# Kernel optimization log

Hardware: AMD Instinct MI355X
Metric: run time of the kernel (lower is better)

## Reference

```python
import jax, jax.numpy as jnp
import numpy as np
import math

NUM_HEADS = 8
EPS = 1e-12  # torch F.normalize eps


def setup_inputs() -> dict:
    key = jax.random.key(0)
    ks = jax.random.split(key, 11)
    b, t, l, c = 2, 8, 1024, 256
    s = 0.02
    return {
        "q": jax.random.normal(ks[0], (b, t, l, c), jnp.float32),
        "k": jax.random.normal(ks[1], (b, t, l, c), jnp.float32),
        "v": jax.random.normal(ks[2], (b, t, l, c), jnp.float32),
        "Wq": jax.random.normal(ks[3], (c, c), jnp.float32) * s,
        "bq": jax.random.normal(ks[4], (c,), jnp.float32) * s,
        "Wk": jax.random.normal(ks[5], (c, c), jnp.float32) * s,
        "bk": jax.random.normal(ks[6], (c,), jnp.float32) * s,
        "Wv": jax.random.normal(ks[7], (c, c), jnp.float32) * s,
        "bv": jax.random.normal(ks[8], (c,), jnp.float32) * s,
        "Wm": jax.random.normal(ks[9], (c, c), jnp.float32) * s,
        "bm": jax.random.normal(ks[10], (c,), jnp.float32) * s,
    }


def _proj_norm(x, W, bias, h, d):
    # Linear (torch: x @ W.T + b), split heads, L2-normalize over head_dim.
    b_, t_, l_, c_ = x.shape
    y = (x @ W.T + bias).reshape(b_, t_, l_, h, d).transpose(0, 1, 3, 2, 4)  # [b,t,h,l,d]
    n = jnp.maximum(jnp.linalg.norm(y, axis=-1, keepdims=True), EPS)
    return y / n


def reference(q, k, v, Wq, bq, Wk, bk, Wv, bv, Wm, bm):
    b, t, l, c = q.shape
    h = NUM_HEADS
    d = c // h
    shortcut = q
    qn = _proj_norm(q, Wq, bq, h, d)  # [b,t,h,l,d]
    kn = _proj_norm(k, Wk, bk, h, d)
    vn = _proj_norm(v, Wv, bv, h, d)
    scores = jnp.einsum('bthqd,bthkd->bthqk', qn, kn) / math.sqrt(d)
    attn = jax.nn.softmax(scores, axis=-1)
    x = jnp.einsum('bthqk,bthkd->bthqd', attn, vn)  # [b,t,h,l,d]
    x = x.transpose(0, 1, 3, 2, 4).reshape(b, t, l, c)
    return x @ Wm.T + bm + shortcut
```

## Files before the change

### kernel.cpp

```cpp
#include <hip/hip_runtime.h>
#include <hip/hip_bf16.h>


#define NTOK  16384
#define CDIM  256
#define LSEQ  1024
#define HEADS 8
#define DHEAD 32

typedef _Float16 f16;
typedef __attribute__((ext_vector_type(2))) _Float16 f16x2;
typedef __attribute__((ext_vector_type(4))) _Float16 f16x4;
typedef __attribute__((ext_vector_type(8))) _Float16 f16x8;
typedef __attribute__((ext_vector_type(4))) float f32x4;
typedef __attribute__((ext_vector_type(16))) float f32x16;

#define QSCALE (0.17677669529663687f * 1.4426950408889634f)

__device__ __forceinline__ f16x2 pkcvt(float a, float b) {
  auto r = __builtin_amdgcn_cvt_pkrtz(a, b);
  union { decltype(r) in; f16x2 out; } u;
  u.in = r;
  return u.out;
}

__device__ __forceinline__ f16x4 pack4(float4 a) {
  union { f16x4 v; f16x2 h[2]; } u;
  u.h[0] = pkcvt(a.x, a.y);
  u.h[1] = pkcvt(a.z, a.w);
  return u.v;
}

__global__ __launch_bounds__(256)
void cvt_w_kernel(const float* __restrict__ Wq, const float* __restrict__ Wk,
                  const float* __restrict__ Wv, const float* __restrict__ Wm,
                  f16* __restrict__ dst) {
  const int m = blockIdx.x >> 6;
  const float* src = (m == 0) ? Wq : (m == 1) ? Wk : (m == 2) ? Wv : Wm;
  const int base = (blockIdx.x & 63) * 1024 + threadIdx.x * 4;
  const int och = base >> 8, ch = base & 255;
  float4 a = *(const float4*)(src + base);
  *(f16x4*)(dst + m * 65536 + (ch >> 5) * 8192 + och * 32 + (ch & 31)) =
      pack4(a);
}

#define PKKB 1288

__global__ __launch_bounds__(256, 2)
void proj_mfma_kernel(const float* __restrict__ xq, const float* __restrict__ xk,
                      const float* __restrict__ xv, const f16* __restrict__ w16,
                      const float* __restrict__ bq, const float* __restrict__ bk,
                      const float* __restrict__ bv,
                      f16* __restrict__ qn, f16* __restrict__ kn,
                      f16* __restrict__ vt) {
  __shared__ f16 xl[8 * PKKB];
  const int which = blockIdx.y;
  const float* x    = (which == 0) ? xq : (which == 1) ? xk : xv;
  const float* bias = (which == 0) ? bq : (which == 1) ? bk : bv;
  const f16* W      = w16 + which * 65536;
  f16* out          = (which == 0) ? qn : (which == 1) ? kn : vt;
  const float scale = (which == 0) ? QSCALE : 1.0f;
  const bool transposed = (which == 2);

  const int tid = threadIdx.x;
  const int wave = tid >> 6, lane = tid & 63;
  const int quad = lane >> 4, l16 = lane & 15;
  const int tokbase = blockIdx.x * 32;
  const int wbase = wave * 64;

  {
    const int c16 = lane;
#pragma unroll
    for (int r = 0; r < 8; ++r) {
      const int tok = r * 4 + wave;
      float4 a = *(const float4*)(x + (size_t)(tokbase + tok) * CDIM + c16 * 4);
      *(f16x4*)(&xl[(c16 >> 3) * PKKB + tok * 40 + (c16 & 7) * 4]) = pack4(a);
    }
  }
  __syncthreads();

  f32x4 acc[4][2];
#pragma unroll
  for (int mt = 0; mt < 4; ++mt)
#pragma unroll
    for (int nt = 0; nt < 2; ++nt) acc[mt][nt] = (f32x4){0.f, 0.f, 0.f, 0.f};

#pragma unroll
  for (int kk = 0; kk < 8; ++kk) {
    f16x8 af[4];
#pragma unroll
    for (int mt = 0; mt < 4; ++mt)
      af[mt] = *(const f16x8*)(W + kk * 8192 + (wbase + mt * 16 + l16) * 32 +
                               quad * 8);
    f16x8 bf0 = *(const f16x8*)(&xl[kk * PKKB + l16 * 40 + quad * 8]);
    f16x8 bf1 = *(const f16x8*)(&xl[kk * PKKB + (16 + l16) * 40 + quad * 8]);
#pragma unroll
    for (int mt = 0; mt < 4; ++mt) {
      acc[mt][0] = __builtin_amdgcn_mfma_f32_16x16x32_f16(af[mt], bf0,
                                                          acc[mt][0], 0, 0, 0);
      acc[mt][1] = __builtin_amdgcn_mfma_f32_16x16x32_f16(af[mt], bf1,
                                                          acc[mt][1], 0, 0, 0);
    }
  }

  const int bt = tokbase >> 10, l0 = tokbase & 1023;
#pragma unroll
  for (int hh = 0; hh < 2; ++hh) {
    const int h = wave * 2 + hh;
    const size_t hb = (size_t)(bt * HEADS + h) * (LSEQ * DHEAD);
    float4 b0 = *(const float4*)(bias + wbase + hh * 32 + quad * 4);
    float4 b1 = *(const float4*)(bias + wbase + hh * 32 + 16 + quad * 4);
#pragma unroll
    for (int nt = 0; nt < 2; ++nt) {
      f32x4 a0 = acc[hh * 2 + 0][nt];
      f32x4 a1 = acc[hh * 2 + 1][nt];
      float v0[4], v1[4];
      v0[0] = a0[0] + b0.x; v0[1] = a0[1] + b0.y;
      v0[2] = a0[2] + b0.z; v0[3] = a0[3] + b0.w;
      v1[0] = a1[0] + b1.x; v1[1] = a1[1] + b1.y;
      v1[2] = a1[2] + b1.z; v1[3] = a1[3] + b1.w;
      float ss = 0.f;
#pragma unroll
      for (int r = 0; r < 4; ++r) ss += v0[r] * v0[r] + v1[r] * v1[r];
      ss += __shfl_xor(ss, 16);
      ss += __shfl_xor(ss, 32);
      const float inv = scale / fmaxf(sqrtf(ss), 1e-12f);
      const int tok_l = l0 + nt * 16 + l16;
      if (!transposed) {
        f16x4 o0, o1;
#pragma unroll
        for (int r = 0; r < 4; ++r) {
          o0[r] = (f16)(v0[r] * inv);
          o1[r] = (f16)(v1[r] * inv);
        }
        *(f16x4*)(out + hb + (size_t)tok_l * DHEAD + quad * 4) = o0;
        *(f16x4*)(out + hb + (size_t)tok_l * DHEAD + 16 + quad * 4) = o1;
      } else {
        const int tcol = (tok_l & ~12) | ((tok_l & 4) << 1) | ((tok_l & 8) >> 1);
#pragma unroll
        for (int r = 0; r < 4; ++r) {
          out[hb + (size_t)(quad * 4 + r) * LSEQ + tcol] = (f16)(v0[r] * inv);
          out[hb + (size_t)(16 + quad * 4 + r) * LSEQ + tcol] = (f16)(v1[r] * inv);
        }
      }
    }
  }
}

#define TKROW 40
#define TVROW 72

__global__ __launch_bounds__(256, 4)
void attn_mfma_kernel(const f16* __restrict__ qn,
                      const f16* __restrict__ kn,
                      const f16* __restrict__ vt,
                      f16* __restrict__ xo) {
  __shared__ f16 kl[2][64 * TKROW];
  __shared__ f16 vl[2][32 * TVROW];
  const int tid  = threadIdx.x;
  const int wave = tid >> 6, lane = tid & 63;
  const int l32 = lane & 31, hi = lane >> 5;
  const int wid = (blockIdx.x & 7) * 128 + (blockIdx.x >> 3);
  const int bth = wid >> 3;
  const int qbase = ((wid & 7) << 7) + wave * 32;
  const size_t hb = (size_t)bth * (LSEQ * DHEAD);

  const f16* qp = qn + hb + (size_t)(qbase + l32) * DHEAD + hi * 8;
  const f16x8 qf0 = *(const f16x8*)qp;
  const f16x8 qf1 = *(const f16x8*)(qp + 16);

  const int krow_w = wave * 16 + (lane >> 2), kcol = (lane & 3) * 8;
  const int vrow_w = wave * 8 + (lane >> 3), vcol = (lane & 7) * 8;
  const f16* gK = kn + hb + (size_t)krow_w * DHEAD + kcol;
  const f16* gV = vt + hb + (size_t)vrow_w * LSEQ + vcol;
  const int lK = krow_w * TKROW + kcol;
  const int lV = vrow_w * TVROW + vcol;

  f32x16 oacc, z16;
#pragma unroll
  for (int r = 0; r < 16; ++r) { oacc[r] = 0.f; z16[r] = 0.f; }
  float ls0 = 0.f, ls1 = 0.f;

#define EXPPV(s, v0, v1) { \
    union { f16x8 v; f16x2 h[4]; } _q0, _q1; \
    _Pragma("unroll") \
    for (int i = 0; i < 4; ++i) { \
      float e0 = __builtin_amdgcn_exp2f(s[2 * i]); \
      float e1 = __builtin_amdgcn_exp2f(s[2 * i + 1]); \
      ls0 += e0; ls1 += e1; \
      _q0.h[i] = pkcvt(e0, e1); \
      float e2 = __builtin_amdgcn_exp2f(s[8 + 2 * i]); \
      float e3 = __builtin_amdgcn_exp2f(s[9 + 2 * i]); \
      ls0 += e2; ls1 += e3; \
      _q1.h[i] = pkcvt(e2, e3); \
    } \
    oacc = __builtin_amdgcn_mfma_f32_32x32x16_f16(v0, _q0.v, oacc, 0, 0, 0); \
    oacc = __builtin_amdgcn_mfma_f32_32x32x16_f16(v1, _q1.v, oacc, 0, 0, 0); }

  f16x8 gk = *(const f16x8*)gK;
  f16x8 gv = *(const f16x8*)gV;
  *(f16x8*)(&kl[0][lK]) = gk;
  *(f16x8*)(&vl[0][lV]) = gv;
  gk = *(const f16x8*)(gK + 64 * DHEAD);
  gv = *(const f16x8*)(gV + 64);
  __syncthreads();

  for (int t = 0; t < 16; ++t) {
    const f16* kb = kl[t & 1];
    const f16* vb = vl[t & 1];
#pragma unroll
    for (int sub = 0; sub < 2; ++sub) {
      f16x8 kf0 = *(const f16x8*)(kb + (sub * 32 + l32) * TKROW + hi * 8);
      f16x8 kf1 = *(const f16x8*)(kb + (sub * 32 + l32) * TKROW + hi * 8 + 16);
      f16x8 vf0 = *(const f16x8*)(vb + l32 * TVROW + sub * 32 + hi * 8);
      f16x8 vf1 = *(const f16x8*)(vb + l32 * TVROW + sub * 32 + hi * 8 + 16);
      f32x16 s = __builtin_amdgcn_mfma_f32_32x32x16_f16(kf0, qf0, z16, 0, 0, 0);
      s = __builtin_amdgcn_mfma_f32_32x32x16_f16(kf1, qf1, s, 0, 0, 0);
      EXPPV(s, vf0, vf1)
    }
    if (t < 15) {
      __syncthreads();
      *(f16x8*)(&kl[(t + 1) & 1][lK]) = gk;
      *(f16x8*)(&vl[(t + 1) & 1][lV]) = gv;
      if (t + 1 < 15) {
        gk = *(const f16x8*)(gK + (size_t)(t + 2) * 64 * DHEAD);
        gv = *(const f16x8*)(gV + (t + 2) * 64);
      }
      __syncthreads();
    }
  }
#undef EXPPV

  float lsum = ls0 + ls1;
  lsum += __shfl_xor(lsum, 32);
  const float inv = __builtin_amdgcn_rcpf(lsum);

  f16* op = xo + hb + (size_t)(qbase + l32) * DHEAD + hi * 4;
#pragma unroll
  for (int g = 0; g < 4; ++g) {
    union { f16x4 v; f16x2 h[2]; } o;
    o.h[0] = pkcvt(oacc[4 * g + 0] * inv, oacc[4 * g + 1] * inv);
    o.h[1] = pkcvt(oacc[4 * g + 2] * inv, oacc[4 * g + 3] * inv);
    *(f16x4*)(op + 8 * g) = o.v;
  }
}

#define OKKB 1288

__global__ __launch_bounds__(256, 2)
void out_proj_mfma_kernel(const f16* __restrict__ xatt,
                          const f16* __restrict__ wm16,
                          const float* __restrict__ bm,
                          const float* __restrict__ resid,
                          float* __restrict__ out) {
  __shared__ f16 xl[8 * OKKB];
  const int tid = threadIdx.x;
  const int wave = tid >> 6, lane = tid & 63;
  const int quad = lane >> 4, l16 = lane & 15;
  const int tokbase = blockIdx.x * 32;
  const int wbase = wave * 64;
  const int bt = tokbase >> 10, l0 = tokbase & 1023;

  {
#pragma unroll
    for (int r = 0; r < 4; ++r) {
      const int flat = r * 256 + tid;
      const int kk = flat >> 7, rem = flat & 127;
      const int tok = rem >> 2, c8 = rem & 3;
      const f16* gp = xatt + (size_t)(bt * HEADS + kk) * (LSEQ * DHEAD) +
                      (size_t)(l0 + tok) * DHEAD + c8 * 8;
      *(f16x8*)(&xl[kk * OKKB + tok * 40 + c8 * 8]) = *(const f16x8*)gp;
    }
  }
  __syncthreads();

  f32x4 acc[4][2];
#pragma unroll
  for (int mt = 0; mt < 4; ++mt)
#pragma unroll
    for (int nt = 0; nt < 2; ++nt) acc[mt][nt] = (f32x4){0.f, 0.f, 0.f, 0.f};

#pragma unroll
  for (int kk = 0; kk < 8; ++kk) {
    f16x8 af[4];
#pragma unroll
    for (int mt = 0; mt < 4; ++mt)
      af[mt] = *(const f16x8*)(wm16 + kk * 8192 +
                               (wbase + mt * 16 + l16) * 32 + quad * 8);
    f16x8 bf0 = *(const f16x8*)(&xl[kk * OKKB + l16 * 40 + quad * 8]);
    f16x8 bf1 = *(const f16x8*)(&xl[kk * OKKB + (16 + l16) * 40 + quad * 8]);
#pragma unroll
    for (int mt = 0; mt < 4; ++mt) {
      acc[mt][0] = __builtin_amdgcn_mfma_f32_16x16x32_f16(af[mt], bf0,
                                                          acc[mt][0], 0, 0, 0);
      acc[mt][1] = __builtin_amdgcn_mfma_f32_16x16x32_f16(af[mt], bf1,
                                                          acc[mt][1], 0, 0, 0);
    }
  }

#pragma unroll
  for (int mt = 0; mt < 4; ++mt) {
    float4 bv = *(const float4*)(bm + wbase + mt * 16 + quad * 4);
#pragma unroll
    for (int nt = 0; nt < 2; ++nt) {
      const int tok = tokbase + nt * 16 + l16;
      const size_t off = (size_t)tok * CDIM + wbase + mt * 16 + quad * 4;
      float4 rv = *(const float4*)(resid + off);
      float4 o;
      o.x = acc[mt][nt][0] + bv.x + rv.x;
      o.y = acc[mt][nt][1] + bv.y + rv.y;
      o.z = acc[mt][nt][2] + bv.z + rv.z;
      o.w = acc[mt][nt][3] + bv.w + rv.w;
      *(float4*)(out + off) = o;
    }
  }
}

extern "C" void kernel_launch(void* const* d_in, const int* in_sizes, int n_in,
                              void* d_out, int out_size, void* d_ws,
                              size_t ws_size, hipStream_t stream) {
  const float* q  = (const float*)d_in[0];
  const float* k  = (const float*)d_in[1];
  const float* v  = (const float*)d_in[2];
  const float* Wq = (const float*)d_in[3];
  const float* bq = (const float*)d_in[4];
  const float* Wk = (const float*)d_in[5];
  const float* bk = (const float*)d_in[6];
  const float* Wv = (const float*)d_in[7];
  const float* bv = (const float*)d_in[8];
  const float* Wm = (const float*)d_in[9];
  const float* bm = (const float*)d_in[10];
  float* outp = (float*)d_out;

  f16* ws = (f16*)d_ws;
  const size_t TENS = (size_t)NTOK * CDIM;
  f16* qn  = ws;
  f16* kn  = ws + TENS;
  f16* vt  = ws + 2 * TENS;
  f16* w16 = ws + 3 * TENS;
  f16* xa  = qn;

  dim3 blk(256);
  cvt_w_kernel<<<dim3(256), blk, 0, stream>>>(Wq, Wk, Wv, Wm, w16);
  proj_mfma_kernel<<<dim3(512, 3), blk, 0, stream>>>(q, k, v, w16, bq, bk, bv,
                                                     qn, kn, vt);
  attn_mfma_kernel<<<dim3(1024), blk, 0, stream>>>(qn, kn, vt, xa);
  out_proj_mfma_kernel<<<dim3(512), blk, 0, stream>>>(xa, w16 + 3 * 65536, bm,
                                                      q, outp);
}
```

Baseline: 156.6 us.

## Split attention keys across waves with direct global loads and LDS reduction

Reworks the attention kernel so each block handles 64 queries and each of its four waves processes a quarter of the keys (256) for both 32-query halves. K and V fragments are read directly from global memory into registers with software double-buffering, replacing the shared-memory staging and its per-tile barriers. Partial outputs and row sums are combined through LDS at the end. This removes barrier stalls and reuses each K/V fragment across two query tiles. The cost is extra LDS use, a final reduction step, twice as many blocks and a lower occupancy bound. No running max is subtracted before the exponentials, which relies on the scores being bounded by the normalized inputs.

```diff
diff --git a/kernel.cpp b/kernel.cpp
--- a/kernel.cpp
+++ b/kernel.cpp
@@ -147,101 +147,124 @@
   }
 }
 
-#define TKROW 40
-#define TVROW 72
-
-__global__ __launch_bounds__(256, 4)
+__global__ __launch_bounds__(256, 2)
 void attn_mfma_kernel(const f16* __restrict__ qn,
                       const f16* __restrict__ kn,
                       const f16* __restrict__ vt,
                       f16* __restrict__ xo) {
-  __shared__ f16 kl[2][64 * TKROW];
-  __shared__ f16 vl[2][32 * TVROW];
+  __shared__ float parr[4][2][64][17];
   const int tid  = threadIdx.x;
   const int wave = tid >> 6, lane = tid & 63;
   const int l32 = lane & 31, hi = lane >> 5;
-  const int wid = (blockIdx.x & 7) * 128 + (blockIdx.x >> 3);
-  const int bth = wid >> 3;
-  const int qbase = ((wid & 7) << 7) + wave * 32;
+  const int wid = (blockIdx.x & 7) * 256 + (blockIdx.x >> 3);
+  const int bth = wid >> 4;
+  const int qbase = (wid & 15) << 6;
   const size_t hb = (size_t)bth * (LSEQ * DHEAD);
 
-  const f16* qp = qn + hb + (size_t)(qbase + l32) * DHEAD + hi * 8;
-  const f16x8 qf0 = *(const f16x8*)qp;
-  const f16x8 qf1 = *(const f16x8*)(qp + 16);
-
-  const int krow_w = wave * 16 + (lane >> 2), kcol = (lane & 3) * 8;
-  const int vrow_w = wave * 8 + (lane >> 3), vcol = (lane & 7) * 8;
-  const f16* gK = kn + hb + (size_t)krow_w * DHEAD + kcol;
-  const f16* gV = vt + hb + (size_t)vrow_w * LSEQ + vcol;
-  const int lK = krow_w * TKROW + kcol;
-  const int lV = vrow_w * TVROW + vcol;
-
-  f32x16 oacc, z16;
-#pragma unroll
-  for (int r = 0; r < 16; ++r) { oacc[r] = 0.f; z16[r] = 0.f; }
-  float ls0 = 0.f, ls1 = 0.f;
-
-#define EXPPV(s, v0, v1) { \
+  const f16* qpA = qn + hb + (size_t)(qbase + l32) * DHEAD + hi * 8;
+  const f16x8 qfA0 = *(const f16x8*)qpA;
+  const f16x8 qfA1 = *(const f16x8*)(qpA + 16);
+  const f16* qpB = qpA + 32 * DHEAD;
+  const f16x8 qfB0 = *(const f16x8*)qpB;
+  const f16x8 qfB1 = *(const f16x8*)(qpB + 16);
+
+  const int k0 = wave * 256;
+  const f16* kB = kn + hb + (size_t)(k0 + l32) * DHEAD + hi * 8;
+  const f16* vB = vt + hb + (size_t)l32 * LSEQ + k0 + hi * 8;
+
+  f32x16 oaccA, oaccB, z16;
+#pragma unroll
+  for (int r = 0; r < 16; ++r) { oaccA[r] = 0.f; oaccB[r] = 0.f; z16[r] = 0.f; }
+  float lsA0 = 0.f, lsA1 = 0.f, lsB0 = 0.f, lsB1 = 0.f;
+
+#define EXPPV(s, v0, v1, oacc, la, lb) { \
     union { f16x8 v; f16x2 h[4]; } _q0, _q1; \
     _Pragma("unroll") \
     for (int i = 0; i < 4; ++i) { \
       float e0 = __builtin_amdgcn_exp2f(s[2 * i]); \
       float e1 = __builtin_amdgcn_exp2f(s[2 * i + 1]); \
-      ls0 += e0; ls1 += e1; \
+      la += e0; lb += e1; \
       _q0.h[i] = pkcvt(e0, e1); \
       float e2 = __builtin_amdgcn_exp2f(s[8 + 2 * i]); \
       float e3 = __builtin_amdgcn_exp2f(s[9 + 2 * i]); \
-      ls0 += e2; ls1 += e3; \
+      la += e2; lb += e3; \
       _q1.h[i] = pkcvt(e2, e3); \
     } \
     oacc = __builtin_amdgcn_mfma_f32_32x32x16_f16(v0, _q0.v, oacc, 0, 0, 0); \
     oacc = __builtin_amdgcn_mfma_f32_32x32x16_f16(v1, _q1.v, oacc, 0, 0, 0); }
 
-  f16x8 gk = *(const f16x8*)gK;
-  f16x8 gv = *(const f16x8*)gV;
-  *(f16x8*)(&kl[0][lK]) = gk;
-  *(f16x8*)(&vl[0][lV]) = gv;
-  gk = *(const f16x8*)(gK + 64 * DHEAD);
-  gv = *(const f16x8*)(gV + 64);
+#define COMPUTE(K0, K1, V0, V1) { \
+    f32x16 sA = __builtin_amdgcn_mfma_f32_32x32x16_f16(K0, qfA0, z16, 0, 0, 0); \
+    sA = __builtin_amdgcn_mfma_f32_32x32x16_f16(K1, qfA1, sA, 0, 0, 0); \
+    EXPPV(sA, V0, V1, oaccA, lsA0, lsA1) \
+    f32x16 sB = __builtin_amdgcn_mfma_f32_32x32x16_f16(K0, qfB0, z16, 0, 0, 0); \
+    sB = __builtin_amdgcn_mfma_f32_32x32x16_f16(K1, qfB1, sB, 0, 0, 0); \
+    EXPPV(sB, V0, V1, oaccB, lsB0, lsB1) }
+
+  f16x8 ka0 = *(const f16x8*)kB;
+  f16x8 ka1 = *(const f16x8*)(kB + 16);
+  f16x8 va0 = *(const f16x8*)vB;
+  f16x8 va1 = *(const f16x8*)(vB + 16);
+  f16x8 kb0_, kb1_, vb0_, vb1_;
+
+  for (int t = 0; t < 8; t += 2) {
+    {
+      const f16* kp = kB + (size_t)(t + 1) * 32 * DHEAD;
+      const f16* vp = vB + (t + 1) * 32;
+      kb0_ = *(const f16x8*)kp;
+      kb1_ = *(const f16x8*)(kp + 16);
+      vb0_ = *(const f16x8*)vp;
+      vb1_ = *(const f16x8*)(vp + 16);
+    }
+    __builtin_amdgcn_s_setprio(1);
+    COMPUTE(ka0, ka1, va0, va1)
+    __builtin_amdgcn_s_setprio(0);
+    if (t + 2 < 8) {
+      const f16* kp = kB + (size_t)(t + 2) * 32 * DHEAD;
+      const f16* vp = vB + (t + 2) * 32;
+      ka0 = *(const f16x8*)kp;
+      ka1 = *(const f16x8*)(kp + 16);
+      va0 = *(const f16x8*)vp;
+      va1 = *(const f16x8*)(vp + 16);
+    }
+    __builtin_amdgcn_s_setprio(1);
+    COMPUTE(kb0_, kb1_, vb0_, vb1_)
+    __builtin_amdgcn_s_setprio(0);
+  }
+#undef COMPUTE
+#undef EXPPV
+
+  const float lsA = lsA0 + lsA1;
+  const float lsB = lsB0 + lsB1;
+#pragma unroll
+  for (int r = 0; r < 16; ++r) {
+    parr[wave][0][lane][r] = oaccA[r];
+    parr[wave][1][lane][r] = oaccB[r];
+  }
+  parr[wave][0][lane][16] = lsA;
+  parr[wave][1][lane][16] = lsB;
   __syncthreads();
 
-  for (int t = 0; t < 16; ++t) {
-    const f16* kb = kl[t & 1];
-    const f16* vb = vl[t & 1];
-#pragma unroll
-    for (int sub = 0; sub < 2; ++sub) {
-      f16x8 kf0 = *(const f16x8*)(kb + (sub * 32 + l32) * TKROW + hi * 8);
-      f16x8 kf1 = *(const f16x8*)(kb + (sub * 32 + l32) * TKROW + hi * 8 + 16);
-      f16x8 vf0 = *(const f16x8*)(vb + l32 * TVROW + sub * 32 + hi * 8);
-      f16x8 vf1 = *(const f16x8*)(vb + l32 * TVROW + sub * 32 + hi * 8 + 16);
-      f32x16 s = __builtin_amdgcn_mfma_f32_32x32x16_f16(kf0, qf0, z16, 0, 0, 0);
-      s = __builtin_amdgcn_mfma_f32_32x32x16_f16(kf1, qf1, s, 0, 0, 0);
-      EXPPV(s, vf0, vf1)
-    }
-    if (t < 15) {
-      __syncthreads();
-      *(f16x8*)(&kl[(t + 1) & 1][lK]) = gk;
-      *(f16x8*)(&vl[(t + 1) & 1][lV]) = gv;
-      if (t + 1 < 15) {
-        gk = *(const f16x8*)(gK + (size_t)(t + 2) * 64 * DHEAD);
-        gv = *(const f16x8*)(gV + (t + 2) * 64);
-      }
-      __syncthreads();
-    }
-  }
-#undef EXPPV
-
-  float lsum = ls0 + ls1;
-  lsum += __shfl_xor(lsum, 32);
-  const float inv = __builtin_amdgcn_rcpf(lsum);
-
-  f16* op = xo + hb + (size_t)(qbase + l32) * DHEAD + hi * 4;
-#pragma unroll
-  for (int g = 0; g < 4; ++g) {
-    union { f16x4 v; f16x2 h[2]; } o;
-    o.h[0] = pkcvt(oacc[4 * g + 0] * inv, oacc[4 * g + 1] * inv);
-    o.h[1] = pkcvt(oacc[4 * g + 2] * inv, oacc[4 * g + 3] * inv);
-    *(f16x4*)(op + 8 * g) = o.v;
+  if (wave < 2) {
+    const int grp = wave;
+    f32x16 oacc;
+    float ls;
+#pragma unroll
+    for (int r = 0; r < 16; ++r)
+      oacc[r] = parr[0][grp][lane][r] + parr[1][grp][lane][r] +
+                parr[2][grp][lane][r] + parr[3][grp][lane][r];
+    ls = parr[0][grp][lane][16] + parr[1][grp][lane][16] +
+         parr[2][grp][lane][16] + parr[3][grp][lane][16];
+    ls += __shfl_xor(ls, 32);
+    const float inv = __builtin_amdgcn_rcpf(ls);
+    f16* op = xo + hb + (size_t)(qbase + grp * 32 + l32) * DHEAD + hi * 4;
+#pragma unroll
+    for (int g = 0; g < 4; ++g) {
+      union { f16x4 v; f16x2 h[2]; } o;
+      o.h[0] = pkcvt(oacc[4 * g + 0] * inv, oacc[4 * g + 1] * inv);
+      o.h[1] = pkcvt(oacc[4 * g + 2] * inv, oacc[4 * g + 3] * inv);
+      *(f16x4*)(op + 8 * g) = o.v;
+    }
   }
 }
 
@@ -344,7 +367,7 @@
   cvt_w_kernel<<<dim3(256), blk, 0, stream>>>(Wq, Wk, Wv, Wm, w16);
   proj_mfma_kernel<<<dim3(512, 3), blk, 0, stream>>>(q, k, v, w16, bq, bk, bv,
                                                      qn, kn, vt);
-  attn_mfma_kernel<<<dim3(1024), blk, 0, stream>>>(qn, kn, vt, xa);
+  attn_mfma_kernel<<<dim3(2048), blk, 0, stream>>>(qn, kn, vt, xa);
   out_proj_mfma_kernel<<<dim3(512), blk, 0, stream>>>(xa, w16 + 3 * 65536, bm,
                                                       q, outp);
 }
```

After: 161.6 us. +3.2%, slower.
